# Performance work log

Hardware: AMD Instinct MI355X
Metric: run time of the kernel (lower is better)

The kernel has to match this reference:

```python
import jax, jax.numpy as jnp
import numpy as np

INPUT_DIM, HIDDEN_DIM, OUTPUT_DIM = 13, 256, 80


def setup_inputs() -> dict:
    key = jax.random.key(0)
    ks = jax.random.split(key, 5)
    x = jax.random.normal(ks[0], (64, 2048, INPUT_DIM), dtype=jnp.float32)
    # Xavier-uniform init like init_weights(); biases zero.
    def xavier(k, fan_in, fan_out):
        lim = np.sqrt(6.0 / (fan_in + fan_out)).astype(np.float32)
        return jax.random.uniform(k, (fan_in, fan_out), jnp.float32, -lim, lim)
    W1 = xavier(ks[1], INPUT_DIM, HIDDEN_DIM)
    W2 = xavier(ks[2], HIDDEN_DIM, HIDDEN_DIM)
    W3 = xavier(ks[3], HIDDEN_DIM, HIDDEN_DIM)
    W4 = xavier(ks[4], HIDDEN_DIM, OUTPUT_DIM)
    b1 = jnp.zeros((HIDDEN_DIM,), jnp.float32)
    b2 = jnp.zeros((HIDDEN_DIM,), jnp.float32)
    b3 = jnp.zeros((HIDDEN_DIM,), jnp.float32)
    b4 = jnp.zeros((OUTPUT_DIM,), jnp.float32)
    return {"x": x, "W1": W1, "b1": b1, "W2": W2, "b2": b2,
            "W3": W3, "b3": b3, "W4": W4, "b4": b4}


def reference(x, W1, b1, W2, b2, W3, b3, W4, b4):
    # Original loops over timesteps, but each timestep is an identical
    # Linear+ReLU stack -> collapse batch*seq into one batched matmul chain.
    h = jax.nn.relu(jnp.einsum('bsi,ih->bsh', x, W1) + b1)   # encoder L1
    h = jax.nn.relu(jnp.einsum('bsh,hk->bsk', h, W2) + b2)   # encoder L2
    h = jax.nn.relu(jnp.einsum('bsh,hk->bsk', h, W3) + b3)   # decoder L1
    out = jnp.einsum('bsh,ho->bso', h, W4) + b4              # decoder L2 (no ReLU)
    return out
```

## Files before the change

kernel.cpp:

```cpp
#include <hip/hip_runtime.h>


typedef _Float16 half_t;
typedef _Float16 half8 __attribute__((ext_vector_type(8)));
typedef float f32x16 __attribute__((ext_vector_type(16)));
typedef unsigned int uint4v __attribute__((ext_vector_type(4)));
typedef int int2v __attribute__((ext_vector_type(2)));

#define M_TOTAL (64*2048)

__global__ void prep_w(const float* __restrict__ W1, const float* __restrict__ W2,
                       const float* __restrict__ W3, const float* __restrict__ W4,
                       half_t* __restrict__ wp) {
    int tid = blockIdx.x * 256 + threadIdx.x;
    if (tid >= 312 * 512) return;
    int blk = tid >> 9, r = tid & 511;
    int lane = r >> 3, j = r & 7;
    const float* W; int K, N, nt, ks;
    if (blk < 8)        { W = W1; K = 13;  N = 256; nt = blk;              ks = 0; }
    else if (blk < 136) { W = W2; K = 256; N = 256; nt = (blk-8) >> 4;     ks = (blk-8) & 15; }
    else if (blk < 264) { W = W3; K = 256; N = 256; nt = (blk-136) >> 4;   ks = (blk-136) & 15; }
    else                { W = W4; K = 256; N = 80;  nt = (blk-264) >> 4;   ks = (blk-264) & 15; }
    int k = ks * 16 + (lane >> 5) * 8 + j;
    int n = nt * 32 + (lane & 31);
    float v = (k < K && n < N) ? W[k * N + n] : 0.f;
    wp[tid] = (half_t)v;
}


__device__ __forceinline__ unsigned int pkrtz(float a, float b) {
    auto p = __builtin_amdgcn_cvt_pkrtz(a, b);
    return __builtin_bit_cast(unsigned int, p);
}

typedef const __attribute__((address_space(1))) unsigned int guint_t;
typedef __attribute__((address_space(3))) unsigned int luint_t;

__device__ __forceinline__ void stage_strip(const half_t* __restrict__ g,
                                            half_t* l, int bytes, int tid) {
    const char* gc = (const char*)g;
    char* lc = (char*)l;
    const int go = tid * 16;
    const int lo = (tid >> 6) << 10;
#pragma unroll
    for (int r = 0; r < bytes; r += 4096) {
        __builtin_amdgcn_global_load_lds((guint_t*)(gc + r + go),
                                         (luint_t*)(lc + r + lo), 16, 0, 0);
    }
}

__device__ __forceinline__ int strip_off(int s) {
    if (s == 0)  return 0;
    if (s <= 4)  return (8   + (s - 1) * 32) * 512;
    if (s <= 8)  return (136 + (s - 5) * 32) * 512;
    if (s == 9)  return 264 * 512;
    return 296 * 512;
}
__device__ __forceinline__ int strip_bytes(int s) {
    return (s == 0) ? 8192 : (s == 10 ? 16384 : 32768);
}

template <int NKS, bool RELU>
__device__ __forceinline__ void dense_tile(const half_t* astrip,
                                           const unsigned int (&Bin)[16][4],
                                           unsigned int (*Bout)[4],
                                           const float* biasnt, int lane, bool hi)
{
    f32x16 acc = {};
    __builtin_amdgcn_s_setprio(1);
#pragma unroll
    for (int ks = 0; ks < NKS; ++ks) {
        half8 a = *(const half8*)(astrip + ((ks * 64 + lane) << 3));
        uint4v bw = { Bin[ks][0], Bin[ks][1], Bin[ks][2], Bin[ks][3] };
        acc = __builtin_amdgcn_mfma_f32_32x32x16_f16(a, __builtin_bit_cast(half8, bw),
                                                     acc, 0, 0, 0);
    }
    __builtin_amdgcn_s_setprio(0);
#pragma unroll
    for (int s = 0; s < 2; ++s) {
        float v[8];
#pragma unroll
        for (int q = 0; q < 8; ++q) {
            int f = (q & 3) + 8 * (q >> 2) + (hi ? 4 : 0);
            float t = acc[8 * s + q] + biasnt[16 * s + f];
            v[q] = RELU ? fmaxf(t, 0.f) : t;
        }
        unsigned int P0 = pkrtz(v[0], v[1]);
        unsigned int P1 = pkrtz(v[2], v[3]);
        unsigned int P2 = pkrtz(v[4], v[5]);
        unsigned int P3 = pkrtz(v[6], v[7]);
        int2v r02 = __builtin_amdgcn_permlane32_swap((int)P0, (int)P2, false, false);
        int2v r13 = __builtin_amdgcn_permlane32_swap((int)P1, (int)P3, false, false);
        Bout[s][0] = (unsigned int)r02.x;
        Bout[s][1] = (unsigned int)r13.x;
        Bout[s][2] = (unsigned int)r02.y;
        Bout[s][3] = (unsigned int)r13.y;
    }
}

__device__ __forceinline__ void out_tile(const half_t* astrip,
                                         const unsigned int (&Bin)[16][4],
                                         const float* biasnt, float* __restrict__ out,
                                         int m0, int nt, int lane, bool hi)
{
    f32x16 acc = {};
    __builtin_amdgcn_s_setprio(1);
#pragma unroll
    for (int ks = 0; ks < 16; ++ks) {
        half8 a = *(const half8*)(astrip + ((ks * 64 + lane) << 3));
        uint4v bw = { Bin[ks][0], Bin[ks][1], Bin[ks][2], Bin[ks][3] };
        acc = __builtin_amdgcn_mfma_f32_32x32x16_f16(a, __builtin_bit_cast(half8, bw),
                                                     acc, 0, 0, 0);
    }
    __builtin_amdgcn_s_setprio(0);
    float* orow = out + (long)(m0 + (lane & 31)) * 80 + nt * 32;
#pragma unroll
    for (int reg = 0; reg < 16; ++reg) {
        if (nt == 2 && (reg >> 2) >= 2) continue;
        int rr = (reg & 3) + 8 * (reg >> 2) + (hi ? 4 : 0);
        orow[rr] = acc[reg] + biasnt[rr];
    }
}

__global__ __launch_bounds__(256, 2) void mlp_mfma(
    const float* __restrict__ x, const half_t* __restrict__ wp,
    const float* __restrict__ b1, const float* __restrict__ b2,
    const float* __restrict__ b3, const float* __restrict__ b4,
    float* __restrict__ out)
{
    __shared__ half_t wbuf[2][16384];
    __shared__ float  bias_lds[864];

    const int tid  = threadIdx.x;
    const int lane = tid & 63;
    const bool hi  = lane >= 32;
    const int m0   = (blockIdx.x * 4 + (tid >> 6)) * 32;

    stage_strip(wp + strip_off(0), wbuf[0], 8192, tid);

    bias_lds[tid] = b1[tid];
    bias_lds[256 + tid] = b2[tid];
    bias_lds[512 + tid] = b3[tid];
    if (tid < 96) bias_lds[768 + tid] = (tid < 80) ? b4[tid] : 0.f;

    unsigned int BA[16][4], BB[16][4];

    {
        const float* xp = x + (long)(m0 + (lane & 31)) * 13;
        float xv[8];
        if (!hi) {
#pragma unroll
            for (int j = 0; j < 8; ++j) xv[j] = xp[j];
        } else {
#pragma unroll
            for (int j = 0; j < 5; ++j) xv[j] = xp[8 + j];
            xv[5] = xv[6] = xv[7] = 0.f;
        }
        BA[0][0] = pkrtz(xv[0], xv[1]);
        BA[0][1] = pkrtz(xv[2], xv[3]);
        BA[0][2] = pkrtz(xv[4], xv[5]);
        BA[0][3] = pkrtz(xv[6], xv[7]);
    }

    __syncthreads();

    stage_strip(wp + strip_off(1), wbuf[1], 32768, tid);
    __builtin_amdgcn_sched_barrier(0);
#pragma unroll
    for (int nt = 0; nt < 8; ++nt)
        dense_tile<1, true>(&wbuf[0][nt * 512], BA, &BB[2 * nt],
                            bias_lds + nt * 32, lane, hi);
    __syncthreads();

#pragma unroll
    for (int p = 1; p <= 4; ++p) {
        if (p < 10) {
            stage_strip(wp + strip_off(p + 1), wbuf[(p + 1) & 1], strip_bytes(p + 1), tid);
            __builtin_amdgcn_sched_barrier(0);
        }
        const half_t* sb = &wbuf[p & 1][0];
#pragma unroll
        for (int sub = 0; sub < 2; ++sub) {
            const int nt = (p - 1) * 2 + sub;
            dense_tile<16, true>(sb + sub * 16 * 512, BB, &BA[2 * nt],
                                 bias_lds + 256 + nt * 32, lane, hi);
        }
        __syncthreads();
    }

#pragma unroll
    for (int p = 5; p <= 8; ++p) {
        stage_strip(wp + strip_off(p + 1), wbuf[(p + 1) & 1], strip_bytes(p + 1), tid);
        __builtin_amdgcn_sched_barrier(0);
        const half_t* sb = &wbuf[p & 1][0];
#pragma unroll
        for (int sub = 0; sub < 2; ++sub) {
            const int nt = (p - 5) * 2 + sub;
            dense_tile<16, true>(sb + sub * 16 * 512, BA, &BB[2 * nt],
                                 bias_lds + 512 + nt * 32, lane, hi);
        }
        __syncthreads();
    }

    stage_strip(wp + strip_off(10), wbuf[0], 16384, tid);
    __builtin_amdgcn_sched_barrier(0);
#pragma unroll
    for (int sub = 0; sub < 2; ++sub)
        out_tile(&wbuf[1][sub * 16 * 512], BB, bias_lds + 768 + sub * 32,
                 out, m0, sub, lane, hi);
    __syncthreads();

    out_tile(&wbuf[0][0], BB, bias_lds + 768 + 64, out, m0, 2, lane, hi);
}


extern "C" void kernel_launch(void* const* d_in, const int* in_sizes, int n_in,
                              void* d_out, int out_size, void* d_ws, size_t ws_size,
                              hipStream_t stream) {
    const float* x  = (const float*)d_in[0];
    const float* W1 = (const float*)d_in[1];
    const float* b1 = (const float*)d_in[2];
    const float* W2 = (const float*)d_in[3];
    const float* b2 = (const float*)d_in[4];
    const float* W3 = (const float*)d_in[5];
    const float* b3 = (const float*)d_in[6];
    const float* W4 = (const float*)d_in[7];
    const float* b4 = (const float*)d_in[8];
    float* out = (float*)d_out;

    half_t* wp = (half_t*)d_ws;

    hipLaunchKernelGGL(prep_w, dim3(624), dim3(256), 0, stream, W1, W2, W3, W4, wp);
    hipLaunchKernelGGL(mlp_mfma, dim3(M_TOTAL / 128), dim3(256), 0, stream,
                       x, wp, b1, b2, b3, b4, out);
}
```

Baseline: 55.09 us.

## Process 64 rows per wave with 2x2 MFMA tiles and loop over two halves

Each wave now computes 64 rows instead of 32, and each block handles 512 rows in two sequential halves, so the grid shrinks by 4x. Every A fragment loaded from LDS feeds two MFMAs, and each weight strip staged into LDS is reused by twice as many rows. This cuts LDS reads and global weight restaging per row. In exchange, register use roughly doubles (two 16x4 activation arrays per buffer and four accumulators), occupancy drops to one wave per EU, and there are only 256 blocks, so parallelism and latency hiding may suffer.

Result: slower. 60.58 us (+10.0%).

```diff
diff --git a/kernel.cpp b/kernel.cpp
--- a/kernel.cpp
+++ b/kernel.cpp
@@ -56,73 +56,131 @@
     if (s == 9)  return 264 * 512;
     return 296 * 512;
 }
-__device__ __forceinline__ int strip_bytes(int s) {
-    return (s == 0) ? 8192 : (s == 10 ? 16384 : 32768);
-}
-
-template <int NKS, bool RELU>
-__device__ __forceinline__ void dense_tile(const half_t* astrip,
-                                           const unsigned int (&Bin)[16][4],
-                                           unsigned int (*Bout)[4],
-                                           const float* biasnt, int lane, bool hi)
-{
-    f32x16 acc = {};
+
+template <bool RELU>
+__device__ __forceinline__ void repack_s(const f32x16& acc, int s,
+                                         const float* biasnt, bool hi,
+                                         unsigned int* Bw)
+{
+    float v[8];
+#pragma unroll
+    for (int q = 0; q < 8; ++q) {
+        int f = (q & 3) + 8 * (q >> 2) + (hi ? 4 : 0);
+        float t = acc[8 * s + q] + biasnt[16 * s + f];
+        v[q] = RELU ? fmaxf(t, 0.f) : t;
+    }
+    unsigned int P0 = pkrtz(v[0], v[1]);
+    unsigned int P1 = pkrtz(v[2], v[3]);
+    unsigned int P2 = pkrtz(v[4], v[5]);
+    unsigned int P3 = pkrtz(v[6], v[7]);
+    int2v r02 = __builtin_amdgcn_permlane32_swap((int)P0, (int)P2, false, false);
+    int2v r13 = __builtin_amdgcn_permlane32_swap((int)P1, (int)P3, false, false);
+    Bw[0] = (unsigned int)r02.x;
+    Bw[1] = (unsigned int)r13.x;
+    Bw[2] = (unsigned int)r02.y;
+    Bw[3] = (unsigned int)r13.y;
+}
+
+#define MFMA16(a, b, c) __builtin_amdgcn_mfma_f32_32x32x16_f16((a), (b), (c), 0, 0, 0)
+
+__device__ __forceinline__ half8 bw_cast(const unsigned int* w) {
+    uint4v t = { w[0], w[1], w[2], w[3] };
+    return __builtin_bit_cast(half8, t);
+}
+
+template <bool RELU>
+__device__ __forceinline__ void dense_phase(const half_t* sb,
+                                            const unsigned int (&Bin)[2][16][4],
+                                            unsigned int (&Bout)[2][16][4],
+                                            int ntbase, const float* biasL,
+                                            int lane, bool hi)
+{
+    f32x16 acc00 = {}, acc01 = {}, acc10 = {}, acc11 = {};
     __builtin_amdgcn_s_setprio(1);
 #pragma unroll
-    for (int ks = 0; ks < NKS; ++ks) {
-        half8 a = *(const half8*)(astrip + ((ks * 64 + lane) << 3));
-        uint4v bw = { Bin[ks][0], Bin[ks][1], Bin[ks][2], Bin[ks][3] };
-        acc = __builtin_amdgcn_mfma_f32_32x32x16_f16(a, __builtin_bit_cast(half8, bw),
-                                                     acc, 0, 0, 0);
+    for (int ks = 0; ks < 16; ++ks) {
+        half8 a0 = *(const half8*)(sb + ((ks * 64 + lane) << 3));
+        half8 a1 = *(const half8*)(sb + 16 * 512 + ((ks * 64 + lane) << 3));
+        half8 b0 = bw_cast(Bin[0][ks]);
+        half8 b1 = bw_cast(Bin[1][ks]);
+        acc00 = MFMA16(a0, b0, acc00);
+        acc01 = MFMA16(a0, b1, acc01);
+        acc10 = MFMA16(a1, b0, acc10);
+        acc11 = MFMA16(a1, b1, acc11);
     }
     __builtin_amdgcn_s_setprio(0);
 #pragma unroll
     for (int s = 0; s < 2; ++s) {
-        float v[8];
-#pragma unroll
-        for (int q = 0; q < 8; ++q) {
-            int f = (q & 3) + 8 * (q >> 2) + (hi ? 4 : 0);
-            float t = acc[8 * s + q] + biasnt[16 * s + f];
-            v[q] = RELU ? fmaxf(t, 0.f) : t;
-        }
-        unsigned int P0 = pkrtz(v[0], v[1]);
-        unsigned int P1 = pkrtz(v[2], v[3]);
-        unsigned int P2 = pkrtz(v[4], v[5]);
-        unsigned int P3 = pkrtz(v[6], v[7]);
-        int2v r02 = __builtin_amdgcn_permlane32_swap((int)P0, (int)P2, false, false);
-        int2v r13 = __builtin_amdgcn_permlane32_swap((int)P1, (int)P3, false, false);
-        Bout[s][0] = (unsigned int)r02.x;
-        Bout[s][1] = (unsigned int)r13.x;
-        Bout[s][2] = (unsigned int)r02.y;
-        Bout[s][3] = (unsigned int)r13.y;
-    }
-}
-
-__device__ __forceinline__ void out_tile(const half_t* astrip,
-                                         const unsigned int (&Bin)[16][4],
-                                         const float* biasnt, float* __restrict__ out,
-                                         int m0, int nt, int lane, bool hi)
-{
-    f32x16 acc = {};
+        repack_s<RELU>(acc00, s, biasL + ntbase * 32, hi, Bout[0][2 * ntbase + s]);
+        repack_s<RELU>(acc01, s, biasL + ntbase * 32, hi, Bout[1][2 * ntbase + s]);
+        repack_s<RELU>(acc10, s, biasL + (ntbase + 1) * 32, hi, Bout[0][2 * (ntbase + 1) + s]);
+        repack_s<RELU>(acc11, s, biasL + (ntbase + 1) * 32, hi, Bout[1][2 * (ntbase + 1) + s]);
+    }
+}
+
+__device__ __forceinline__ void out_phase2(const half_t* sb,
+                                           const unsigned int (&Bin)[2][16][4],
+                                           const float* bias4, float* __restrict__ out,
+                                           int mb, int lane, bool hi)
+{
+    f32x16 acc00 = {}, acc01 = {}, acc10 = {}, acc11 = {};
     __builtin_amdgcn_s_setprio(1);
 #pragma unroll
     for (int ks = 0; ks < 16; ++ks) {
-        half8 a = *(const half8*)(astrip + ((ks * 64 + lane) << 3));
-        uint4v bw = { Bin[ks][0], Bin[ks][1], Bin[ks][2], Bin[ks][3] };
-        acc = __builtin_amdgcn_mfma_f32_32x32x16_f16(a, __builtin_bit_cast(half8, bw),
-                                                     acc, 0, 0, 0);
+        half8 a0 = *(const half8*)(sb + ((ks * 64 + lane) << 3));
+        half8 a1 = *(const half8*)(sb + 16 * 512 + ((ks * 64 + lane) << 3));
+        half8 b0 = bw_cast(Bin[0][ks]);
+        half8 b1 = bw_cast(Bin[1][ks]);
+        acc00 = MFMA16(a0, b0, acc00);
+        acc01 = MFMA16(a0, b1, acc01);
+        acc10 = MFMA16(a1, b0, acc10);
+        acc11 = MFMA16(a1, b1, acc11);
     }
     __builtin_amdgcn_s_setprio(0);
-    float* orow = out + (long)(m0 + (lane & 31)) * 80 + nt * 32;
-#pragma unroll
-    for (int reg = 0; reg < 16; ++reg) {
-        if (nt == 2 && (reg >> 2) >= 2) continue;
-        int rr = (reg & 3) + 8 * (reg >> 2) + (hi ? 4 : 0);
-        orow[rr] = acc[reg] + biasnt[rr];
-    }
-}
-
-__global__ __launch_bounds__(256, 2) void mlp_mfma(
+#pragma unroll
+    for (int ntL = 0; ntL < 2; ++ntL) {
+#pragma unroll
+        for (int g = 0; g < 2; ++g) {
+            const f32x16& acc = ntL == 0 ? (g == 0 ? acc00 : acc01)
+                                         : (g == 0 ? acc10 : acc11);
+            float* orow = out + (long)(mb + g * 32 + (lane & 31)) * 80 + ntL * 32;
+#pragma unroll
+            for (int reg = 0; reg < 16; ++reg) {
+                int rr = (reg & 3) + 8 * (reg >> 2) + (hi ? 4 : 0);
+                orow[rr] = acc[reg] + bias4[ntL * 32 + rr];
+            }
+        }
+    }
+}
+
+__device__ __forceinline__ void out_phase1(const half_t* sb,
+                                           const unsigned int (&Bin)[2][16][4],
+                                           const float* bias42, float* __restrict__ out,
+                                           int mb, int lane, bool hi)
+{
+    f32x16 acc0 = {}, acc1 = {};
+    __builtin_amdgcn_s_setprio(1);
+#pragma unroll
+    for (int ks = 0; ks < 16; ++ks) {
+        half8 a = *(const half8*)(sb + ((ks * 64 + lane) << 3));
+        acc0 = MFMA16(a, bw_cast(Bin[0][ks]), acc0);
+        acc1 = MFMA16(a, bw_cast(Bin[1][ks]), acc1);
+    }
+    __builtin_amdgcn_s_setprio(0);
+#pragma unroll
+    for (int g = 0; g < 2; ++g) {
+        const f32x16& acc = g == 0 ? acc0 : acc1;
+        float* orow = out + (long)(mb + g * 32 + (lane & 31)) * 80 + 64;
+#pragma unroll
+        for (int reg = 0; reg < 8; ++reg) {
+            int rr = (reg & 3) + 8 * (reg >> 2) + (hi ? 4 : 0);
+            orow[rr] = acc[reg] + bias42[rr];
+        }
+    }
+}
+
+__global__ __attribute__((amdgpu_flat_work_group_size(256, 256), amdgpu_waves_per_eu(1)))
+void mlp_mfma(
     const float* __restrict__ x, const half_t* __restrict__ wp,
     const float* __restrict__ b1, const float* __restrict__ b2,
     const float* __restrict__ b3, const float* __restrict__ b4,
@@ -133,8 +191,8 @@
 
     const int tid  = threadIdx.x;
     const int lane = tid & 63;
+    const int wave = tid >> 6;
     const bool hi  = lane >= 32;
-    const int m0   = (blockIdx.x * 4 + (tid >> 6)) * 32;
 
     stage_strip(wp + strip_off(0), wbuf[0], 8192, tid);
 
@@ -143,74 +201,92 @@
     bias_lds[512 + tid] = b3[tid];
     if (tid < 96) bias_lds[768 + tid] = (tid < 80) ? b4[tid] : 0.f;
 
-    unsigned int BA[16][4], BB[16][4];
-
-    {
-        const float* xp = x + (long)(m0 + (lane & 31)) * 13;
-        float xv[8];
-        if (!hi) {
-#pragma unroll
-            for (int j = 0; j < 8; ++j) xv[j] = xp[j];
-        } else {
-#pragma unroll
-            for (int j = 0; j < 5; ++j) xv[j] = xp[8 + j];
-            xv[5] = xv[6] = xv[7] = 0.f;
-        }
-        BA[0][0] = pkrtz(xv[0], xv[1]);
-        BA[0][1] = pkrtz(xv[2], xv[3]);
-        BA[0][2] = pkrtz(xv[4], xv[5]);
-        BA[0][3] = pkrtz(xv[6], xv[7]);
-    }
-
     __syncthreads();
 
-    stage_strip(wp + strip_off(1), wbuf[1], 32768, tid);
-    __builtin_amdgcn_sched_barrier(0);
-#pragma unroll
-    for (int nt = 0; nt < 8; ++nt)
-        dense_tile<1, true>(&wbuf[0][nt * 512], BA, &BB[2 * nt],
-                            bias_lds + nt * 32, lane, hi);
-    __syncthreads();
-
-#pragma unroll
-    for (int p = 1; p <= 4; ++p) {
-        if (p < 10) {
-            stage_strip(wp + strip_off(p + 1), wbuf[(p + 1) & 1], strip_bytes(p + 1), tid);
+#pragma unroll
+    for (int h = 0; h < 2; ++h) {
+        const int mb = blockIdx.x * 512 + h * 256 + wave * 64;
+
+        unsigned int Bx[2][4];
+#pragma unroll
+        for (int g = 0; g < 2; ++g) {
+            const float* xp = x + (long)(mb + g * 32 + (lane & 31)) * 13;
+            float xv[8];
+            if (!hi) {
+#pragma unroll
+                for (int j = 0; j < 8; ++j) xv[j] = xp[j];
+            } else {
+#pragma unroll
+                for (int j = 0; j < 5; ++j) xv[j] = xp[8 + j];
+                xv[5] = xv[6] = xv[7] = 0.f;
+            }
+            Bx[g][0] = pkrtz(xv[0], xv[1]);
+            Bx[g][1] = pkrtz(xv[2], xv[3]);
+            Bx[g][2] = pkrtz(xv[4], xv[5]);
+            Bx[g][3] = pkrtz(xv[6], xv[7]);
+        }
+
+        unsigned int BA[2][16][4], BB[2][16][4];
+
+        {
+            const int p = h * 11;
+            stage_strip(wp + strip_off(1), wbuf[(p + 1) & 1], 32768, tid);
             __builtin_amdgcn_sched_barrier(0);
-        }
-        const half_t* sb = &wbuf[p & 1][0];
-#pragma unroll
-        for (int sub = 0; sub < 2; ++sub) {
-            const int nt = (p - 1) * 2 + sub;
-            dense_tile<16, true>(sb + sub * 16 * 512, BB, &BA[2 * nt],
-                                 bias_lds + 256 + nt * 32, lane, hi);
-        }
-        __syncthreads();
-    }
-
-#pragma unroll
-    for (int p = 5; p <= 8; ++p) {
-        stage_strip(wp + strip_off(p + 1), wbuf[(p + 1) & 1], strip_bytes(p + 1), tid);
-        __builtin_amdgcn_sched_barrier(0);
-        const half_t* sb = &wbuf[p & 1][0];
-#pragma unroll
-        for (int sub = 0; sub < 2; ++sub) {
-            const int nt = (p - 5) * 2 + sub;
-            dense_tile<16, true>(sb + sub * 16 * 512, BA, &BB[2 * nt],
-                                 bias_lds + 512 + nt * 32, lane, hi);
-        }
-        __syncthreads();
-    }
-
-    stage_strip(wp + strip_off(10), wbuf[0], 16384, tid);
-    __builtin_amdgcn_sched_barrier(0);
-#pragma unroll
-    for (int sub = 0; sub < 2; ++sub)
-        out_tile(&wbuf[1][sub * 16 * 512], BB, bias_lds + 768 + sub * 32,
-                 out, m0, sub, lane, hi);
-    __syncthreads();
-
-    out_tile(&wbuf[0][0], BB, bias_lds + 768 + 64, out, m0, 2, lane, hi);
+            const half_t* sb = &wbuf[p & 1][0];
+            half8 bx0 = bw_cast(Bx[0]);
+            half8 bx1 = bw_cast(Bx[1]);
+#pragma unroll
+            for (int nt = 0; nt < 8; ++nt) {
+                half8 a = *(const half8*)(sb + nt * 512 + (lane << 3));
+                f32x16 acc0 = {}, acc1 = {};
+                acc0 = MFMA16(a, bx0, acc0);
+                acc1 = MFMA16(a, bx1, acc1);
+#pragma unroll
+                for (int s = 0; s < 2; ++s) {
+                    repack_s<true>(acc0, s, bias_lds + nt * 32, hi, BB[0][2 * nt + s]);
+                    repack_s<true>(acc1, s, bias_lds + nt * 32, hi, BB[1][2 * nt + s]);
+                }
+            }
+            __syncthreads();
+        }
+
+#pragma unroll
+        for (int i = 0; i < 4; ++i) {
+            const int p = h * 11 + 1 + i;
+            stage_strip(wp + strip_off(2 + i), wbuf[(p + 1) & 1], 32768, tid);
+            __builtin_amdgcn_sched_barrier(0);
+            dense_phase<true>(&wbuf[p & 1][0], BB, BA, 2 * i, bias_lds + 256, lane, hi);
+            __syncthreads();
+        }
+
+#pragma unroll
+        for (int i = 0; i < 4; ++i) {
+            const int p = h * 11 + 5 + i;
+            stage_strip(wp + strip_off(6 + i), wbuf[(p + 1) & 1],
+                        (6 + i == 9) ? 32768 : 32768, tid);
+            __builtin_amdgcn_sched_barrier(0);
+            dense_phase<true>(&wbuf[p & 1][0], BA, BB, 2 * i, bias_lds + 512, lane, hi);
+            __syncthreads();
+        }
+
+        {
+            const int p = h * 11 + 9;
+            stage_strip(wp + strip_off(10), wbuf[(p + 1) & 1], 16384, tid);
+            __builtin_amdgcn_sched_barrier(0);
+            out_phase2(&wbuf[p & 1][0], BB, bias_lds + 768, out, mb, lane, hi);
+            __syncthreads();
+        }
+
+        {
+            const int p = h * 11 + 10;
+            if (h == 0) {
+                stage_strip(wp + strip_off(0), wbuf[(p + 1) & 1], 8192, tid);
+                __builtin_amdgcn_sched_barrier(0);
+            }
+            out_phase1(&wbuf[p & 1][0], BB, bias_lds + 768 + 64, out, mb, lane, hi);
+            __syncthreads();
+        }
+    }
 }
 
 
@@ -231,6 +307,6 @@
     half_t* wp = (half_t*)d_ws;
 
     hipLaunchKernelGGL(prep_w, dim3(624), dim3(256), 0, stream, W1, W2, W3, W4, wp);
-    hipLaunchKernelGGL(mlp_mfma, dim3(M_TOTAL / 128), dim3(256), 0, stream,
+    hipLaunchKernelGGL(mlp_mfma, dim3(M_TOTAL / 512), dim3(256), 0, stream,
                        x, wp, b1, b2, b3, b4, out);
 }
```
